# Kernel tuning notes

Measured on AMD Instinct MI355X. Metric: run time of the kernel, lower is better.

## Reference

```python
import jax, jax.numpy as jnp
import numpy as np

HEAD_SIZE = 128  # hidden_size 2048 / 16 heads; used only as softmax scale in this module


def setup_inputs() -> dict:
    key = jax.random.key(0)
    ks = jax.random.split(key, 4)
    B, S, H = 2, 4096, 2048
    hidden_states = jax.random.normal(ks[0], (B, S, H), dtype=jnp.float32)
    attention_mask = jnp.zeros((B, 1, S), dtype=jnp.float32)  # additive mask, broadcasts onto [B,S,S]
    s = 1.0 / np.sqrt(H)
    Wq = jax.random.normal(ks[1], (H, H), dtype=jnp.float32) * s
    Wk = jax.random.normal(ks[2], (H, H), dtype=jnp.float32) * s
    Wv = jax.random.normal(ks[3], (H, H), dtype=jnp.float32) * s
    bq = jnp.zeros((H,), dtype=jnp.float32)
    bk = jnp.zeros((H,), dtype=jnp.float32)
    bv = jnp.zeros((H,), dtype=jnp.float32)
    return {"hidden_states": hidden_states, "attention_mask": attention_mask,
            "Wq": Wq, "bq": bq, "Wk": Wk, "bk": bk, "Wv": Wv, "bv": bv}


def reference(hidden_states, attention_mask, Wq, bq, Wk, bk, Wv, bv):
    # Self-attention: cross_hidden_states defaults to hidden_states.
    q = jnp.einsum('bsh,oh->bso', hidden_states, Wq) + bq  # [B,S,H]
    k = jnp.einsum('bsh,oh->bso', hidden_states, Wk) + bk
    v = jnp.einsum('bsh,oh->bso', hidden_states, Wv) + bv
    # Note: module never splits heads, so scores are a single [B,S,S] matrix
    scores = jnp.einsum('bqh,bkh->bqk', q, k) / jnp.sqrt(jnp.asarray(HEAD_SIZE, q.dtype))
    scores = scores + attention_mask  # additive mask, broadcast
    probs = jax.nn.softmax(scores, axis=-1)  # dropout p=0 -> identity
    context = jnp.einsum('bqk,bkh->bqh', probs, v)  # [B,S,H]
    return context
```

## Files before the change

### kernel.cpp

```cpp
#include <hip/hip_runtime.h>

typedef _Float16 f16;
typedef _Float16 f16x8 __attribute__((ext_vector_type(8)));
typedef _Float16 f16x4 __attribute__((ext_vector_type(4)));
typedef float    f32x16 __attribute__((ext_vector_type(16)));

#define GLD16(g, l)                                                            \
  __builtin_amdgcn_global_load_lds(                                            \
      (const __attribute__((address_space(1))) void*)(g),                      \
      (__attribute__((address_space(3))) void*)(l), 16, 0, 0)

static constexpr int S = 4096, H = 2048, B = 2;

__global__ __launch_bounds__(256) void cast_all(
    const float* __restrict__ hs, const float* __restrict__ w0,
    const float* __restrict__ w1, const float* __restrict__ w2,
    f16* __restrict__ hs_h, f16* __restrict__ w_h) {
  const int hsN4 = B * S * H / 4;
  const int wN4  = H * H / 4;
  int i = blockIdx.x * 256 + threadIdx.x;
  float4 f;
  if (i < hsN4) {
    f = reinterpret_cast<const float4*>(hs)[i];
    f16x4 h = {(f16)f.x, (f16)f.y, (f16)f.z, (f16)f.w};
    reinterpret_cast<f16x4*>(hs_h)[i] = h;
  } else {
    int j = i - hsN4;
    int seg = j / wN4, off = j - seg * wN4;
    const float* src = seg == 0 ? w0 : (seg == 1 ? w1 : w2);
    f = reinterpret_cast<const float4*>(src)[off];
    f16x4 h = {(f16)f.x, (f16)f.y, (f16)f.z, (f16)f.w};
    reinterpret_cast<f16x4*>(w_h)[j] = h;
  }
}

template <int MODE>
__global__ __launch_bounds__(512, 2) void gemm_tn(
    const f16* __restrict__ A, const f16* __restrict__ Bm,
    void* __restrict__ C0, void* __restrict__ C1, void* __restrict__ C2,
    const float* __restrict__ x0, const float* __restrict__ x1,
    const float* __restrict__ x2, float scale, int K, int lda, int ldb) {
  __shared__ __attribute__((aligned(16))) char smem[131072];

  const int tileM = blockIdx.y * 256;
  const int tileN = blockIdx.x * 256;

  const int tid  = threadIdx.x;
  const int wave = tid >> 6, lane = tid & 63;
  const int wm = (wave >> 2) * 128;
  const int wn = (wave & 3) * 64;
  const int l31 = lane & 31, khalf = lane >> 5;

  f32x16 acc[4][2] = {};

  size_t rowB = tileN;
  if (MODE == 2) rowB = (size_t)(tileM >> 12) * S + tileN;
  if (MODE == 3) rowB = (size_t)(tileM >> 12) * H + tileN;
  const f16* gA = A + (size_t)tileM * lda;
  const f16* gB = Bm + rowB * ldb;

  int aoff[4], boff[4], loff[4];
#pragma unroll
  for (int j = 0; j < 4; ++j) {
    int id = j * 512 + tid;
    int r = id >> 3, cs = (id & 7) ^ (r & 7) ^ ((r & 16) >> 2);
    aoff[j] = r * lda + cs * 8;
    boff[j] = r * ldb + cs * 8;
    loff[j] = id * 8;
  }

  const int rsw = (l31 & 7) ^ ((l31 & 16) >> 2);
  const int nt = K >> 6;

  {
    f16* pA = (f16*)smem;
    f16* pB = (f16*)(smem + 32768);
#pragma unroll
    for (int j = 0; j < 4; ++j) GLD16(gA + aoff[j], &pA[loff[j]]);
#pragma unroll
    for (int j = 0; j < 4; ++j) GLD16(gB + boff[j], &pB[loff[j]]);
  }
  asm volatile("s_waitcnt vmcnt(0)" ::: "memory");
  __builtin_amdgcn_s_barrier();

  for (int t = 0; t < nt; ++t) {
    const int cur = t & 1;
    const f16* sA = (const f16*)(smem + cur * 65536);
    const f16* sB = (const f16*)(smem + cur * 65536 + 32768);
    const bool pf = (t + 1 < nt);
    if (pf) {
      f16* pA = (f16*)(smem + (cur ^ 1) * 65536);
      f16* pB = (f16*)(smem + (cur ^ 1) * 65536 + 32768);
      const int kg = (t + 1) * 64;
#pragma unroll
      for (int j = 0; j < 4; ++j) GLD16(gA + aoff[j] + kg, &pA[loff[j]]);
#pragma unroll
      for (int j = 0; j < 4; ++j) GLD16(gB + boff[j] + kg, &pB[loff[j]]);
    }
#pragma unroll
    for (int c = 0; c < 4; ++c) {
      const int pos = ((c * 2 + khalf) ^ rsw) * 8;
      f16x8 af[4], bf[2];
#pragma unroll
      for (int x = 0; x < 4; ++x)
        af[x] = *reinterpret_cast<const f16x8*>(&sA[(wm + x * 32 + l31) * 64 + pos]);
#pragma unroll
      for (int y = 0; y < 2; ++y)
        bf[y] = *reinterpret_cast<const f16x8*>(&sB[(wn + y * 32 + l31) * 64 + pos]);
      __builtin_amdgcn_s_setprio(1);
#pragma unroll
      for (int x = 0; x < 4; ++x)
#pragma unroll
        for (int y = 0; y < 2; ++y)
          acc[x][y] = __builtin_amdgcn_mfma_f32_32x32x16_f16(af[x], bf[y], acc[x][y], 0, 0, 0);
      __builtin_amdgcn_s_setprio(0);
    }
    if (pf) asm volatile("s_waitcnt vmcnt(0)" ::: "memory");
    __builtin_amdgcn_s_barrier();
  }

  if (MODE == 0 && (tileN >> 11) == 2) {
    const int nn0 = tileN - 2 * H;
    const int b = tileM >> 12, s0 = tileM & (S - 1);
    f16* sT = (f16*)smem;
#pragma unroll
    for (int p = 0; p < 4; ++p) {
      if ((wave & 3) == p) {
#pragma unroll
        for (int x = 0; x < 4; ++x)
#pragma unroll
          for (int y = 0; y < 2; ++y) {
            int scol = y * 32 + l31;
            float bias = x2[nn0 + p * 64 + scol];
#pragma unroll
            for (int g = 0; g < 4; ++g) {
              int row = wm + x * 32 + g * 8 + khalf * 4;
              f16x4 h4 = {(f16)(acc[x][y][g * 4 + 0] + bias),
                          (f16)(acc[x][y][g * 4 + 1] + bias),
                          (f16)(acc[x][y][g * 4 + 2] + bias),
                          (f16)(acc[x][y][g * 4 + 3] + bias)};
              *reinterpret_cast<f16x4*>(&sT[scol * 264 + row]) = h4;
            }
          }
      }
      __syncthreads();
      {
        int c = tid >> 3, hh = tid & 7;
        const f16* src = &sT[c * 264 + hh * 32];
        f16* dst = (f16*)C2 + (size_t)b * H * S + (size_t)(nn0 + p * 64 + c) * S +
                   s0 + hh * 32;
#pragma unroll
        for (int j = 0; j < 4; ++j)
          reinterpret_cast<f16x8*>(dst)[j] = reinterpret_cast<const f16x8*>(src)[j];
      }
      __syncthreads();
    }
    return;
  }

#pragma unroll
  for (int x = 0; x < 4; ++x)
#pragma unroll
    for (int y = 0; y < 2; ++y)
#pragma unroll
      for (int r = 0; r < 16; ++r) {
        int m = tileM + wm + x * 32 + (r & 3) + 8 * (r >> 2) + 4 * khalf;
        int n = tileN + wn + y * 32 + l31;
        float v = acc[x][y][r];
        if (MODE == 0) {
          int seg = n >> 11, nn = n & 2047;
          if (seg == 0) {
            ((f16*)C0)[(size_t)m * H + nn] = (f16)(v + x0[nn]);
          } else {
            ((f16*)C1)[(size_t)m * H + nn] = (f16)(v + x1[nn]);
          }
        } else if (MODE == 2) {
          int b = m >> 12;
          ((f16*)C0)[(size_t)m * S + n] = (f16)(v * scale + x0[(size_t)b * S + n]);
        } else {
          ((float*)C0)[(size_t)m * H + n] = v;
        }
      }
}

__global__ __launch_bounds__(256) void softmax_f16(f16* __restrict__ sc) {
  const int tid = threadIdx.x;
  f16* rp = sc + (size_t)blockIdx.x * S;
  f16x8 h[2];
#pragma unroll
  for (int j = 0; j < 2; ++j) h[j] = reinterpret_cast<f16x8*>(rp)[tid + j * 256];

  float v[16];
#pragma unroll
  for (int j = 0; j < 2; ++j)
#pragma unroll
    for (int e = 0; e < 8; ++e) v[j * 8 + e] = (float)h[j][e];

  float m = -1e30f;
#pragma unroll
  for (int e = 0; e < 16; ++e) m = fmaxf(m, v[e]);
#pragma unroll
  for (int off = 32; off; off >>= 1) m = fmaxf(m, __shfl_xor(m, off));

  __shared__ float red[8];
  int wave = tid >> 6, lane = tid & 63;
  if (lane == 0) red[wave] = m;
  __syncthreads();
  m = fmaxf(fmaxf(red[0], red[1]), fmaxf(red[2], red[3]));

  float s = 0.f;
#pragma unroll
  for (int e = 0; e < 16; ++e) { v[e] = __expf(v[e] - m); s += v[e]; }
#pragma unroll
  for (int off = 32; off; off >>= 1) s += __shfl_xor(s, off);
  if (lane == 0) red[4 + wave] = s;
  __syncthreads();
  s = red[4] + red[5] + red[6] + red[7];
  float inv = 1.0f / s;

#pragma unroll
  for (int j = 0; j < 2; ++j) {
#pragma unroll
    for (int e = 0; e < 8; ++e) h[j][e] = (f16)(v[j * 8 + e] * inv);
    reinterpret_cast<f16x8*>(rp)[tid + j * 256] = h[j];
  }
}

extern "C" void kernel_launch(void* const* d_in, const int* in_sizes, int n_in,
                              void* d_out, int out_size, void* d_ws, size_t ws_size,
                              hipStream_t stream) {
  const float* hs   = (const float*)d_in[0];
  const float* mask = (const float*)d_in[1];
  const float* Wq   = (const float*)d_in[2];
  const float* bq   = (const float*)d_in[3];
  const float* Wk   = (const float*)d_in[4];
  const float* bk   = (const float*)d_in[5];
  const float* Wv   = (const float*)d_in[6];
  const float* bv   = (const float*)d_in[7];
  float* out = (float*)d_out;

  f16* hs_h = (f16*)d_ws;
  f16* w_h  = hs_h + (size_t)B * S * H;
  f16* Qh   = w_h + (size_t)3 * H * H;
  f16* Kh   = Qh + (size_t)B * S * H;
  f16* Vt   = Kh + (size_t)B * S * H;
  f16* Sc   = Vt + (size_t)B * S * H;

  const int castN = B * S * H / 4 + 3 * H * H / 4;
  cast_all<<<(castN + 255) / 256, 256, 0, stream>>>(hs, Wq, Wk, Wv, hs_h, w_h);

  dim3 blk(512);
  const float sscale = 0.088388347648318447f;

  gemm_tn<0><<<dim3(24, 32), blk, 0, stream>>>(
      hs_h, w_h, Qh, Kh, Vt, bq, bk, bv, 1.f, H, H, H);

  gemm_tn<2><<<dim3(16, 32), blk, 0, stream>>>(
      Qh, Kh, Sc, nullptr, nullptr, mask, nullptr, nullptr, sscale, H, H, H);

  softmax_f16<<<B * S, 256, 0, stream>>>(Sc);

  gemm_tn<3><<<dim3(8, 32), blk, 0, stream>>>(
      Sc, Vt, out, nullptr, nullptr, nullptr, nullptr, nullptr, 1.f, S, S, S);
}
```

Before: 659.4 us.

## Switch GEMM to 16x16x32 MFMA with phased LDS reads and barrier ping-pong

```diff
diff --git a/kernel.cpp b/kernel.cpp
--- a/kernel.cpp
+++ b/kernel.cpp
@@ -3,7 +3,7 @@
 typedef _Float16 f16;
 typedef _Float16 f16x8 __attribute__((ext_vector_type(8)));
 typedef _Float16 f16x4 __attribute__((ext_vector_type(4)));
-typedef float    f32x16 __attribute__((ext_vector_type(16)));
+typedef float    f32x4 __attribute__((ext_vector_type(4)));
 
 #define GLD16(g, l)                                                            \
   __builtin_amdgcn_global_load_lds(                                            \
@@ -49,9 +49,9 @@
   const int wave = tid >> 6, lane = tid & 63;
   const int wm = (wave >> 2) * 128;
   const int wn = (wave & 3) * 64;
-  const int l31 = lane & 31, khalf = lane >> 5;
-
-  f32x16 acc[4][2] = {};
+  const int ln = lane & 15, kq = lane >> 4;
+
+  f32x4 acc[8][4] = {};
 
   size_t rowB = tileN;
   if (MODE == 2) rowB = (size_t)(tileM >> 12) * S + tileN;
@@ -69,8 +69,13 @@
     loff[j] = id * 8;
   }
 
-  const int rsw = (l31 & 7) ^ ((l31 & 16) >> 2);
   const int nt = K >> 6;
+
+  auto rdfrag = [&](const f16* sT, int rbase, int ks) -> f16x8 {
+    const int row = rbase + ln;
+    const int slot = (ks * 4 + kq) ^ (row & 7) ^ ((row & 16) >> 2);
+    return *reinterpret_cast<const f16x8*>(&sT[row * 64 + slot * 8]);
+  };
 
   {
     f16* pA = (f16*)smem;
@@ -87,36 +92,67 @@
     const int cur = t & 1;
     const f16* sA = (const f16*)(smem + cur * 65536);
     const f16* sB = (const f16*)(smem + cur * 65536 + 32768);
+    f16* pA = (f16*)(smem + (cur ^ 1) * 65536);
+    f16* pB = (f16*)(smem + (cur ^ 1) * 65536 + 32768);
+    const int kg = (t + 1) * 64;
     const bool pf = (t + 1 < nt);
+
+    f16x8 bf[2][4];
+
+#pragma unroll
+    for (int ks = 0; ks < 2; ++ks)
+#pragma unroll
+      for (int y = 0; y < 4; ++y) bf[ks][y] = rdfrag(sB, wn + y * 16, ks);
+    f16x8 a00 = rdfrag(sA, wm + 0 * 16, 0), a01 = rdfrag(sA, wm + 0 * 16, 1);
+    f16x8 a10 = rdfrag(sA, wm + 1 * 16, 0), a11 = rdfrag(sA, wm + 1 * 16, 1);
     if (pf) {
-      f16* pA = (f16*)(smem + (cur ^ 1) * 65536);
-      f16* pB = (f16*)(smem + (cur ^ 1) * 65536 + 32768);
-      const int kg = (t + 1) * 64;
 #pragma unroll
       for (int j = 0; j < 4; ++j) GLD16(gA + aoff[j] + kg, &pA[loff[j]]);
 #pragma unroll
       for (int j = 0; j < 4; ++j) GLD16(gB + boff[j] + kg, &pB[loff[j]]);
     }
-#pragma unroll
-    for (int c = 0; c < 4; ++c) {
-      const int pos = ((c * 2 + khalf) ^ rsw) * 8;
-      f16x8 af[4], bf[2];
-#pragma unroll
-      for (int x = 0; x < 4; ++x)
-        af[x] = *reinterpret_cast<const f16x8*>(&sA[(wm + x * 32 + l31) * 64 + pos]);
-#pragma unroll
-      for (int y = 0; y < 2; ++y)
-        bf[y] = *reinterpret_cast<const f16x8*>(&sB[(wn + y * 32 + l31) * 64 + pos]);
+    __builtin_amdgcn_s_barrier();
+    asm volatile("s_waitcnt lgkmcnt(0)" ::: "memory");
+    __builtin_amdgcn_sched_barrier(0);
+    __builtin_amdgcn_s_setprio(1);
+#pragma unroll
+    for (int y = 0; y < 4; ++y) {
+      acc[0][y] = __builtin_amdgcn_mfma_f32_16x16x32_f16(a00, bf[0][y], acc[0][y], 0, 0, 0);
+      acc[1][y] = __builtin_amdgcn_mfma_f32_16x16x32_f16(a10, bf[0][y], acc[1][y], 0, 0, 0);
+    }
+#pragma unroll
+    for (int y = 0; y < 4; ++y) {
+      acc[0][y] = __builtin_amdgcn_mfma_f32_16x16x32_f16(a01, bf[1][y], acc[0][y], 0, 0, 0);
+      acc[1][y] = __builtin_amdgcn_mfma_f32_16x16x32_f16(a11, bf[1][y], acc[1][y], 0, 0, 0);
+    }
+    __builtin_amdgcn_s_setprio(0);
+    __builtin_amdgcn_s_barrier();
+
+#pragma unroll
+    for (int p = 1; p < 4; ++p) {
+      f16x8 b00 = rdfrag(sA, wm + (2 * p + 0) * 16, 0);
+      f16x8 b01 = rdfrag(sA, wm + (2 * p + 0) * 16, 1);
+      f16x8 b10 = rdfrag(sA, wm + (2 * p + 1) * 16, 0);
+      f16x8 b11 = rdfrag(sA, wm + (2 * p + 1) * 16, 1);
+      __builtin_amdgcn_s_barrier();
+      asm volatile("s_waitcnt lgkmcnt(0)" ::: "memory");
+      __builtin_amdgcn_sched_barrier(0);
       __builtin_amdgcn_s_setprio(1);
 #pragma unroll
-      for (int x = 0; x < 4; ++x)
-#pragma unroll
-        for (int y = 0; y < 2; ++y)
-          acc[x][y] = __builtin_amdgcn_mfma_f32_32x32x16_f16(af[x], bf[y], acc[x][y], 0, 0, 0);
+      for (int y = 0; y < 4; ++y) {
+        acc[2 * p + 0][y] = __builtin_amdgcn_mfma_f32_16x16x32_f16(b00, bf[0][y], acc[2 * p + 0][y], 0, 0, 0);
+        acc[2 * p + 1][y] = __builtin_amdgcn_mfma_f32_16x16x32_f16(b10, bf[0][y], acc[2 * p + 1][y], 0, 0, 0);
+      }
+#pragma unroll
+      for (int y = 0; y < 4; ++y) {
+        acc[2 * p + 0][y] = __builtin_amdgcn_mfma_f32_16x16x32_f16(b01, bf[1][y], acc[2 * p + 0][y], 0, 0, 0);
+        acc[2 * p + 1][y] = __builtin_amdgcn_mfma_f32_16x16x32_f16(b11, bf[1][y], acc[2 * p + 1][y], 0, 0, 0);
+      }
       __builtin_amdgcn_s_setprio(0);
-    }
-    if (pf) asm volatile("s_waitcnt vmcnt(0)" ::: "memory");
-    __builtin_amdgcn_s_barrier();
+      if (p == 3 && pf)
+        asm volatile("s_waitcnt vmcnt(0)" ::: "memory");
+      __builtin_amdgcn_s_barrier();
+    }
   }
 
   if (MODE == 0 && (tileN >> 11) == 2) {
@@ -127,20 +163,15 @@
     for (int p = 0; p < 4; ++p) {
       if ((wave & 3) == p) {
 #pragma unroll
-        for (int x = 0; x < 4; ++x)
-#pragma unroll
-          for (int y = 0; y < 2; ++y) {
-            int scol = y * 32 + l31;
+        for (int x = 0; x < 8; ++x)
+#pragma unroll
+          for (int y = 0; y < 4; ++y) {
+            int scol = y * 16 + ln;
             float bias = x2[nn0 + p * 64 + scol];
-#pragma unroll
-            for (int g = 0; g < 4; ++g) {
-              int row = wm + x * 32 + g * 8 + khalf * 4;
-              f16x4 h4 = {(f16)(acc[x][y][g * 4 + 0] + bias),
-                          (f16)(acc[x][y][g * 4 + 1] + bias),
-                          (f16)(acc[x][y][g * 4 + 2] + bias),
-                          (f16)(acc[x][y][g * 4 + 3] + bias)};
-              *reinterpret_cast<f16x4*>(&sT[scol * 264 + row]) = h4;
-            }
+            int row0 = wm + x * 16 + kq * 4;
+            f16x4 h4 = {(f16)(acc[x][y][0] + bias), (f16)(acc[x][y][1] + bias),
+                        (f16)(acc[x][y][2] + bias), (f16)(acc[x][y][3] + bias)};
+            *reinterpret_cast<f16x4*>(&sT[scol * 264 + row0]) = h4;
           }
       }
       __syncthreads();
@@ -159,13 +190,13 @@
   }
 
 #pragma unroll
-  for (int x = 0; x < 4; ++x)
-#pragma unroll
-    for (int y = 0; y < 2; ++y)
-#pragma unroll
-      for (int r = 0; r < 16; ++r) {
-        int m = tileM + wm + x * 32 + (r & 3) + 8 * (r >> 2) + 4 * khalf;
-        int n = tileN + wn + y * 32 + l31;
+  for (int x = 0; x < 8; ++x)
+#pragma unroll
+    for (int y = 0; y < 4; ++y)
+#pragma unroll
+      for (int r = 0; r < 4; ++r) {
+        int m = tileM + wm + x * 16 + kq * 4 + r;
+        int n = tileN + wn + y * 16 + ln;
         float v = acc[x][y][r];
         if (MODE == 0) {
           int seg = n >> 11, nn = n & 2047;
```

After: 630.5 us. 4.4% less time.
